# Kernel tuning notes

Measured on AMD Instinct MI355X. Metric: run time of the kernel, lower is better.

The kernel has to match this reference:

```python
import jax, jax.numpy as jnp
import numpy as np

N_WINDOW = 128  # |i-j| < N_WINDOW kept
D_K = 64

def setup_inputs() -> dict:
    key = jax.random.key(0)
    kq, kk, kv = jax.random.split(key, 3)
    B, H, S, D = 2, 8, 2048, D_K
    Q = jax.random.normal(kq, (B, H, S, D), dtype=jnp.float32)
    K = jax.random.normal(kk, (B, H, S, D), dtype=jnp.float32)
    V = jax.random.normal(kv, (B, H, S, D), dtype=jnp.float32)
    return {"Q": Q, "K": K, "V": V}

def reference(Q, K, V):
    S = Q.shape[-2]
    # scores: [B, H, S, S]
    scores = jnp.einsum('bhqd,bhkd->bhqk', Q, K) / jnp.sqrt(jnp.float32(D_K))
    idx = jnp.arange(S)
    band = jnp.abs(idx[:, None] - idx[None, :]) < N_WINDOW  # [S, S] band mask
    scores = jnp.where(band[None, None, :, :], scores, -jnp.inf)
    attn = jax.nn.softmax(scores, axis=-1)
    context = jnp.einsum('bhqk,bhkd->bhqd', attn, V)
    return (context, attn)
```

## Files before the change

kernel.cpp:

```cpp
#include <hip/hip_runtime.h>
#include <math.h>

#define S_LEN 2048
#define DK 64
#define TQ 32
#define KLW 320
#define NCH 5
#define PSTR 324
#define PSTR4 81

typedef __attribute__((ext_vector_type(8))) short bf16x8;
typedef __attribute__((ext_vector_type(4))) float f32x4;

__device__ __forceinline__ short f2bf(float f) {
    unsigned u = __float_as_uint(f);
    unsigned r = (u + 0x7fffu + ((u >> 16) & 1u)) >> 16;
    return (short)r;
}

__device__ __forceinline__ bf16x8 pack8(f32x4 a, f32x4 b) {
    bf16x8 r;
    r[0] = f2bf(a[0]); r[1] = f2bf(a[1]); r[2] = f2bf(a[2]); r[3] = f2bf(a[3]);
    r[4] = f2bf(b[0]); r[5] = f2bf(b[1]); r[6] = f2bf(b[2]); r[7] = f2bf(b[3]);
    return r;
}

__global__ __launch_bounds__(256, 3) void band_attn_v4(
    const float* __restrict__ Q,
    const float* __restrict__ K,
    const float* __restrict__ V,
    float* __restrict__ ctx_out,
    float* __restrict__ attn_out)
{
    __shared__ __align__(16) float Ps[TQ * PSTR];

    const int tid  = threadIdx.x;
    const int bh   = blockIdx.x >> 6;
    const int q0   = (blockIdx.x & 63) * TQ;
    const int base = q0 - 128;

    const int lane = tid & 63;
    const int wv   = tid >> 6;
    const int col  = lane & 15;
    const int quad = lane >> 4;

    const float* Qh = Q + ((size_t)bh * S_LEN + q0) * DK;
    const float* Kh = K + (size_t)bh * S_LEN * DK;
    const float* Vh = V + (size_t)bh * S_LEN * DK;

    bf16x8 qf[2][2];
    #pragma unroll
    for (int qt = 0; qt < 2; ++qt)
        #pragma unroll
        for (int h = 0; h < 2; ++h) {
            const float* qp = Qh + (size_t)(16 * qt + col) * DK + 32 * h + 8 * quad;
            f32x4 a = *(const f32x4*)qp;
            f32x4 b = *(const f32x4*)(qp + 4);
            a *= 0.125f; b *= 0.125f;
            qf[qt][h] = pack8(a, b);
        }

    #pragma unroll
    for (int c = 0; c < NCH; ++c) {
        const int kl  = c * 64 + 16 * wv + col;
        const int kg  = base + kl;
        const int kgc = min(max(kg, 0), S_LEN - 1);
        bf16x8 kf[2];
        #pragma unroll
        for (int h = 0; h < 2; ++h) {
            const float* kp = Kh + (size_t)kgc * DK + 32 * h + 8 * quad;
            kf[h] = pack8(*(const f32x4*)kp, *(const f32x4*)(kp + 4));
        }
        #pragma unroll
        for (int qt = 0; qt < 2; ++qt) {
            f32x4 acc = {0.f, 0.f, 0.f, 0.f};
            acc = __builtin_amdgcn_mfma_f32_16x16x32_bf16(qf[qt][0], kf[0], acc, 0, 0, 0);
            acc = __builtin_amdgcn_mfma_f32_16x16x32_bf16(qf[qt][1], kf[1], acc, 0, 0, 0);
            #pragma unroll
            for (int r = 0; r < 4; ++r) {
                const int qloc = 16 * qt + quad * 4 + r;
                const bool ok = ((unsigned)kg < S_LEN) && (kl > qloc) && (kl <= qloc + 255);
                Ps[qloc * PSTR + kl] = ok ? acc[r] : -INFINITY;
            }
        }
    }
    __syncthreads();

    #pragma unroll
    for (int rr = 0; rr < 8; ++rr) {
        float* row = Ps + (wv * 8 + rr) * PSTR;
        float v[5];
        #pragma unroll
        for (int j = 0; j < 5; ++j) v[j] = row[lane + 64 * j];
        float m = fmaxf(fmaxf(fmaxf(v[0], v[1]), fmaxf(v[2], v[3])), v[4]);
        #pragma unroll
        for (int off = 32; off > 0; off >>= 1) m = fmaxf(m, __shfl_xor(m, off, 64));
        float e[5], sum = 0.f;
        #pragma unroll
        for (int j = 0; j < 5; ++j) { e[j] = __expf(v[j] - m); sum += e[j]; }
        #pragma unroll
        for (int off = 32; off > 0; off >>= 1) sum += __shfl_xor(sum, off, 64);
        const float inv = 1.0f / sum;
        #pragma unroll
        for (int j = 0; j < 5; ++j) row[lane + 64 * j] = e[j] * inv;
    }
    __syncthreads();

    f32x4 o0 = {0.f, 0.f, 0.f, 0.f}, o1 = {0.f, 0.f, 0.f, 0.f};
    const float* vcol = Vh + 16 * wv + col;
    #pragma unroll
    for (int c = 0; c < NCH; ++c) {
        #pragma unroll
        for (int h = 0; h < 2; ++h) {
            const int k0 = base + c * 64 + 32 * h + 8 * quad;
            f32x4 va, vb;
            #pragma unroll
            for (int j = 0; j < 4; ++j) {
                int kgc = min(max(k0 + j, 0), S_LEN - 1);
                va[j] = vcol[(size_t)kgc * DK];
            }
            #pragma unroll
            for (int j = 0; j < 4; ++j) {
                int kgc = min(max(k0 + 4 + j, 0), S_LEN - 1);
                vb[j] = vcol[(size_t)kgc * DK];
            }
            bf16x8 vf = pack8(va, vb);
            #pragma unroll
            for (int qt = 0; qt < 2; ++qt) {
                const float* pp = Ps + (size_t)(16 * qt + col) * PSTR + c * 64 + 32 * h + 8 * quad;
                bf16x8 pf = pack8(*(const f32x4*)pp, *(const f32x4*)(pp + 4));
                if (qt == 0) o0 = __builtin_amdgcn_mfma_f32_16x16x32_bf16(pf, vf, o0, 0, 0, 0);
                else         o1 = __builtin_amdgcn_mfma_f32_16x16x32_bf16(pf, vf, o1, 0, 0, 0);
            }
        }
    }

    {
        float* Cg = ctx_out + ((size_t)bh * S_LEN + q0) * DK;
        #pragma unroll
        for (int r = 0; r < 4; ++r) {
            Cg[(size_t)(quad * 4 + r) * DK + 16 * wv + col]      = o0[r];
            Cg[(size_t)(16 + quad * 4 + r) * DK + 16 * wv + col] = o1[r];
        }
    }

    {
        const int kloff4 = (q0 >> 2) - 32;
        f32x4* A4 = (f32x4*)(attn_out + ((size_t)bh * S_LEN + q0 + 8 * wv) * S_LEN);
        const f32x4* Ps4 = (const f32x4*)Ps;
        const f32x4 z = {0.f, 0.f, 0.f, 0.f};
        #pragma unroll 8
        for (int i = 0; i < 64; ++i) {
            const int idx  = i * 64 + lane;
            const int r    = idx >> 9;
            const int slot = idx & 511;
            const int kl4  = slot - kloff4;
            f32x4 v = ((unsigned)kl4 < 80u) ? Ps4[(8 * wv + r) * PSTR4 + kl4] : z;
            A4[(size_t)r * 512 + slot] = v;
        }
    }
}

extern "C" void kernel_launch(void* const* d_in, const int* in_sizes, int n_in,
                              void* d_out, int out_size, void* d_ws, size_t ws_size,
                              hipStream_t stream) {
    const float* Q = (const float*)d_in[0];
    const float* K = (const float*)d_in[1];
    const float* V = (const float*)d_in[2];
    float* out = (float*)d_out;

    const int BH = in_sizes[0] / (S_LEN * DK);
    const size_t ctx_elems = (size_t)BH * S_LEN * DK;
    float* ctx  = out;
    float* attn = out + ctx_elems;

    dim3 grid(BH * (S_LEN / TQ));
    band_attn_v4<<<grid, 256, 0, stream>>>(Q, K, V, ctx, attn);
}
```

Baseline: 303.8 us.

## Halve query tile to 16 rows, split attn store into zero/copy loops, use bf16 intrinsics

```diff
diff --git a/kernel.cpp b/kernel.cpp
--- a/kernel.cpp
+++ b/kernel.cpp
@@ -1,9 +1,10 @@
 #include <hip/hip_runtime.h>
+#include <hip/hip_bf16.h>
 #include <math.h>
 
 #define S_LEN 2048
 #define DK 64
-#define TQ 32
+#define TQ 16
 #define KLW 320
 #define NCH 5
 #define PSTR 324
@@ -12,20 +13,16 @@
 typedef __attribute__((ext_vector_type(8))) short bf16x8;
 typedef __attribute__((ext_vector_type(4))) float f32x4;
 
-__device__ __forceinline__ short f2bf(float f) {
-    unsigned u = __float_as_uint(f);
-    unsigned r = (u + 0x7fffu + ((u >> 16) & 1u)) >> 16;
-    return (short)r;
+__device__ __forceinline__ bf16x8 pack8(f32x4 a, f32x4 b) {
+    union { __hip_bfloat162 h[4]; bf16x8 v; } u;
+    u.h[0] = __float22bfloat162_rn(make_float2(a[0], a[1]));
+    u.h[1] = __float22bfloat162_rn(make_float2(a[2], a[3]));
+    u.h[2] = __float22bfloat162_rn(make_float2(b[0], b[1]));
+    u.h[3] = __float22bfloat162_rn(make_float2(b[2], b[3]));
+    return u.v;
 }
 
-__device__ __forceinline__ bf16x8 pack8(f32x4 a, f32x4 b) {
-    bf16x8 r;
-    r[0] = f2bf(a[0]); r[1] = f2bf(a[1]); r[2] = f2bf(a[2]); r[3] = f2bf(a[3]);
-    r[4] = f2bf(b[0]); r[5] = f2bf(b[1]); r[6] = f2bf(b[2]); r[7] = f2bf(b[3]);
-    return r;
-}
-
-__global__ __launch_bounds__(256, 3) void band_attn_v4(
+__global__ __launch_bounds__(256, 4) void band_attn_v5(
     const float* __restrict__ Q,
     const float* __restrict__ K,
     const float* __restrict__ V,
@@ -35,8 +32,8 @@
     __shared__ __align__(16) float Ps[TQ * PSTR];
 
     const int tid  = threadIdx.x;
-    const int bh   = blockIdx.x >> 6;
-    const int q0   = (blockIdx.x & 63) * TQ;
+    const int bh   = blockIdx.x >> 7;
+    const int q0   = (blockIdx.x & 127) << 4;
     const int base = q0 - 128;
 
     const int lane = tid & 63;
@@ -48,17 +45,15 @@
     const float* Kh = K + (size_t)bh * S_LEN * DK;
     const float* Vh = V + (size_t)bh * S_LEN * DK;
 
-    bf16x8 qf[2][2];
+    bf16x8 qf[2];
     #pragma unroll
-    for (int qt = 0; qt < 2; ++qt)
-        #pragma unroll
-        for (int h = 0; h < 2; ++h) {
-            const float* qp = Qh + (size_t)(16 * qt + col) * DK + 32 * h + 8 * quad;
-            f32x4 a = *(const f32x4*)qp;
-            f32x4 b = *(const f32x4*)(qp + 4);
-            a *= 0.125f; b *= 0.125f;
-            qf[qt][h] = pack8(a, b);
-        }
+    for (int h = 0; h < 2; ++h) {
+        const float* qp = Qh + (size_t)col * DK + 32 * h + 8 * quad;
+        f32x4 a = *(const f32x4*)qp;
+        f32x4 b = *(const f32x4*)(qp + 4);
+        a *= 0.125f; b *= 0.125f;
+        qf[h] = pack8(a, b);
+    }
 
     #pragma unroll
     for (int c = 0; c < NCH; ++c) {
@@ -71,24 +66,21 @@
             const float* kp = Kh + (size_t)kgc * DK + 32 * h + 8 * quad;
             kf[h] = pack8(*(const f32x4*)kp, *(const f32x4*)(kp + 4));
         }
+        f32x4 acc = {0.f, 0.f, 0.f, 0.f};
+        acc = __builtin_amdgcn_mfma_f32_16x16x32_bf16(qf[0], kf[0], acc, 0, 0, 0);
+        acc = __builtin_amdgcn_mfma_f32_16x16x32_bf16(qf[1], kf[1], acc, 0, 0, 0);
         #pragma unroll
-        for (int qt = 0; qt < 2; ++qt) {
-            f32x4 acc = {0.f, 0.f, 0.f, 0.f};
-            acc = __builtin_amdgcn_mfma_f32_16x16x32_bf16(qf[qt][0], kf[0], acc, 0, 0, 0);
-            acc = __builtin_amdgcn_mfma_f32_16x16x32_bf16(qf[qt][1], kf[1], acc, 0, 0, 0);
-            #pragma unroll
-            for (int r = 0; r < 4; ++r) {
-                const int qloc = 16 * qt + quad * 4 + r;
-                const bool ok = ((unsigned)kg < S_LEN) && (kl > qloc) && (kl <= qloc + 255);
-                Ps[qloc * PSTR + kl] = ok ? acc[r] : -INFINITY;
-            }
+        for (int r = 0; r < 4; ++r) {
+            const int qloc = quad * 4 + r;
+            const bool ok = ((unsigned)kg < S_LEN) && (kl > qloc) && (kl <= qloc + 255);
+            Ps[qloc * PSTR + kl] = ok ? acc[r] : -INFINITY;
         }
     }
     __syncthreads();
 
     #pragma unroll
-    for (int rr = 0; rr < 8; ++rr) {
-        float* row = Ps + (wv * 8 + rr) * PSTR;
+    for (int rr = 0; rr < 4; ++rr) {
+        float* row = Ps + (wv * 4 + rr) * PSTR;
         float v[5];
         #pragma unroll
         for (int j = 0; j < 5; ++j) v[j] = row[lane + 64 * j];
@@ -106,7 +98,7 @@
     }
     __syncthreads();
 
-    f32x4 o0 = {0.f, 0.f, 0.f, 0.f}, o1 = {0.f, 0.f, 0.f, 0.f};
+    f32x4 o = {0.f, 0.f, 0.f, 0.f};
     const float* vcol = Vh + 16 * wv + col;
     #pragma unroll
     for (int c = 0; c < NCH; ++c) {
@@ -125,38 +117,33 @@
                 vb[j] = vcol[(size_t)kgc * DK];
             }
             bf16x8 vf = pack8(va, vb);
-            #pragma unroll
-            for (int qt = 0; qt < 2; ++qt) {
-                const float* pp = Ps + (size_t)(16 * qt + col) * PSTR + c * 64 + 32 * h + 8 * quad;
-                bf16x8 pf = pack8(*(const f32x4*)pp, *(const f32x4*)(pp + 4));
-                if (qt == 0) o0 = __builtin_amdgcn_mfma_f32_16x16x32_bf16(pf, vf, o0, 0, 0, 0);
-                else         o1 = __builtin_amdgcn_mfma_f32_16x16x32_bf16(pf, vf, o1, 0, 0, 0);
-            }
+            const float* pp = Ps + (size_t)col * PSTR + c * 64 + 32 * h + 8 * quad;
+            bf16x8 pf = pack8(*(const f32x4*)pp, *(const f32x4*)(pp + 4));
+            o = __builtin_amdgcn_mfma_f32_16x16x32_bf16(pf, vf, o, 0, 0, 0);
         }
     }
 
     {
         float* Cg = ctx_out + ((size_t)bh * S_LEN + q0) * DK;
         #pragma unroll
-        for (int r = 0; r < 4; ++r) {
-            Cg[(size_t)(quad * 4 + r) * DK + 16 * wv + col]      = o0[r];
-            Cg[(size_t)(16 + quad * 4 + r) * DK + 16 * wv + col] = o1[r];
-        }
+        for (int r = 0; r < 4; ++r)
+            Cg[(size_t)(quad * 4 + r) * DK + 16 * wv + col] = o[r];
     }
 
     {
         const int kloff4 = (q0 >> 2) - 32;
-        f32x4* A4 = (f32x4*)(attn_out + ((size_t)bh * S_LEN + q0 + 8 * wv) * S_LEN);
+        const int L = max(0, kloff4);
+        const int R = min(512, kloff4 + (KLW >> 2));
+        f32x4* A4 = (f32x4*)(attn_out + ((size_t)bh * S_LEN + q0 + 4 * wv) * S_LEN);
         const f32x4* Ps4 = (const f32x4*)Ps;
         const f32x4 z = {0.f, 0.f, 0.f, 0.f};
-        #pragma unroll 8
-        for (int i = 0; i < 64; ++i) {
-            const int idx  = i * 64 + lane;
-            const int r    = idx >> 9;
-            const int slot = idx & 511;
-            const int kl4  = slot - kloff4;
-            f32x4 v = ((unsigned)kl4 < 80u) ? Ps4[(8 * wv + r) * PSTR4 + kl4] : z;
-            A4[(size_t)r * 512 + slot] = v;
+        #pragma unroll
+        for (int rr = 0; rr < 4; ++rr) {
+            f32x4* row4 = A4 + (size_t)rr * 512;
+            const f32x4* pr = Ps4 + (4 * wv + rr) * PSTR4 - kloff4;
+            for (int s = lane; s < L; s += 64)       row4[s] = z;
+            for (int s = L + lane; s < R; s += 64)   row4[s] = pr[s];
+            for (int s = R + lane; s < 512; s += 64) row4[s] = z;
         }
     }
 }
@@ -175,5 +162,5 @@
     float* attn = out + ctx_elems;
 
     dim3 grid(BH * (S_LEN / TQ));
-    band_attn_v4<<<grid, 256, 0, stream>>>(Q, K, V, ctx, attn);
+    band_attn_v5<<<grid, 256, 0, stream>>>(Q, K, V, ctx, attn);
 }
```

Result: slower. 313.8 us (+3.3%).
